# Performance work log

Hardware: AMD Instinct MI355X
Metric: run time of the kernel (lower is better)

## Reference

```python
import jax, jax.numpy as jnp
import numpy as np
from jax import lax

NUM_SAMPLES = 16
EPSILON = 1e-08
CHUNK = 1024  # tile size for the reverse NN search (matches torch batch_size)


def _cdist(a, b):
    # Euclidean distance matrix [Na, Nb] via gemm form, numerically floored for sqrt.
    d2 = (a * a).sum(-1)[:, None] + (b * b).sum(-1)[None, :] - 2.0 * (a @ b.T)
    return jnp.sqrt(jnp.maximum(d2, 1e-12))


def setup_inputs() -> dict:
    key = jax.random.key(0)
    k = jax.random.split(key, 6)
    N, F, M, G = 16384, 16384, 4096, 8192
    return {
        "original_vertices": jax.random.normal(k[0], (N, 3), dtype=jnp.float32),
        "original_faces": jax.random.randint(k[1], (F, 3), 0, N),
        "simplified_vertices": jax.random.normal(k[2], (M, 3), dtype=jnp.float32),
        "simplified_faces": jax.random.randint(k[3], (G, 3), 0, M),
        "face_probabilities": jax.random.uniform(k[4], (G,), dtype=jnp.float32),
        "r1": jax.random.uniform(k[5], (G, NUM_SAMPLES, 1), dtype=jnp.float32),
        "r2": jax.random.uniform(jax.random.fold_in(key, 7), (G, NUM_SAMPLES, 1), dtype=jnp.float32),
    }


def reference(original_vertices, original_faces, simplified_vertices,
              simplified_faces, face_probabilities, r1, r2):
    G = simplified_faces.shape[0]
    probs = face_probabilities[:G]  # pad/slice to num simplified faces (identity here)

    # ---- forward term: simplified barycenters -> nearest original barycenter ----
    orig_bary = original_vertices[original_faces].mean(axis=1)      # [F,3]
    simp_bary = simplified_vertices[simplified_faces].mean(axis=1)  # [G,3]
    min_d = _cdist(simp_bary, orig_bary).min(axis=1)                # [G]
    forward_term = (probs * min_d).sum() + 1e-4 * (1.0 - probs).sum()

    # ---- reverse term: sample points on simplified faces, NN to original verts ----
    sqrt_r1 = jnp.sqrt(r1)
    u = 1.0 - sqrt_r1
    v = sqrt_r1 * (1.0 - r2)
    w = sqrt_r1 * r2
    fv = simplified_vertices[simplified_faces]  # [G,3,3]
    pts = (u * fv[:, None, 0] + v * fv[:, None, 1] + w * fv[:, None, 2]).reshape(-1, 3)

    total = pts.shape[0]  # G * NUM_SAMPLES, divisible by CHUNK
    vsq = (original_vertices * original_vertices).sum(-1)  # [N]

    def chunk_min(p):  # p: [CHUNK, 3]
        d2 = (p * p).sum(-1)[:, None] + vsq[None, :] - 2.0 * (p @ original_vertices.T)
        return jnp.sqrt(jnp.maximum(d2, 1e-12)).min(axis=1)

    mins = lax.map(chunk_min, pts.reshape(total // CHUNK, CHUNK, 3)).reshape(-1)
    max_dist = mins.max() + EPSILON
    scaled = mins / max_dist * 0.1
    probs_exp = jnp.repeat(probs, NUM_SAMPLES)
    reverse_term = (probs_exp * scaled).sum()

    return forward_term + reverse_term
```

## Files before the change

### kernel.cpp

```cpp
#include <hip/hip_runtime.h>
#include <math.h>

constexpr int N_V  = 16384;
constexpr int N_F  = 16384;
constexpr int G_F  = 8192;
constexpr int NS   = 16;
constexpr int NPTS = G_F * NS;

constexpr int MB    = 2;
constexpr int CT    = 16;

typedef _Float16 half8 __attribute__((ext_vector_type(8)));
typedef float    f32x16 __attribute__((ext_vector_type(16)));

constexpr int F4_ACC   = 0;
constexpr int F4_SB    = 1;
constexpr int F4_PTS   = F4_SB + G_F;
constexpr int F4_PKV   = F4_PTS + NPTS;
constexpr int F4_PKO   = F4_PKV + 32768;
constexpr int F4_TOTAL = F4_PKO + 32768;
constexpr int WS_MINF  = F4_TOTAL * 4;
constexpr int WS_MINR  = WS_MINF + G_F;

__device__ __forceinline__ f32x16 mfma16(half8 a, half8 b, f32x16 c) {
  return __builtin_amdgcn_mfma_f32_32x32x16_f16(a, b, c, 0, 0, 0);
}

__device__ __forceinline__ void pack_target(float x, float y, float z, float sq,
                                            half8* __restrict__ pk, int tile, int n) {
  float ax = -2.0f*x, ay = -2.0f*y, az = -2.0f*z;
  _Float16 hx = (_Float16)ax, hy = (_Float16)ay, hz = (_Float16)az, hw = (_Float16)sq;
  _Float16 lx = (_Float16)(ax - (float)hx), ly = (_Float16)(ay - (float)hy);
  _Float16 lz = (_Float16)(az - (float)hz), lw = (_Float16)(sq - (float)hw);
  half8 h0; h0[0]=hx; h0[1]=hy; h0[2]=hz; h0[3]=hw; h0[4]=lx; h0[5]=ly; h0[6]=lz; h0[7]=lw;
  half8 h1; h1[0]=hx; h1[1]=hy; h1[2]=hz; h1[3]=hw;
  h1[4]=(_Float16)0.0f; h1[5]=(_Float16)0.0f; h1[6]=(_Float16)0.0f; h1[7]=(_Float16)0.0f;
  pk[(size_t)tile*64 + n]      = h0;
  pk[(size_t)tile*64 + 32 + n] = h1;
}

__global__ void k_prep(const float* __restrict__ ov, const int* __restrict__ of,
                       const float* __restrict__ sv, const int* __restrict__ sf,
                       const float* __restrict__ r1, const float* __restrict__ r2,
                       unsigned int* __restrict__ ws, float4* __restrict__ ws4) {
  int i = blockIdx.x * blockDim.x + threadIdx.x;
  if (i < 4) ws[i] = 0u;
  ws[WS_MINR + i] = 0x7f800000u;

  {
    int g = i >> 4;
    int a = sf[3*g], b = sf[3*g+1], c = sf[3*g+2];
    float sr = sqrtf(r1[i]);
    float u = 1.0f - sr;
    float v = sr * (1.0f - r2[i]);
    float w = sr * r2[i];
    float px = u*sv[3*a]   + v*sv[3*b]   + w*sv[3*c];
    float py = u*sv[3*a+1] + v*sv[3*b+1] + w*sv[3*c+1];
    float pz = u*sv[3*a+2] + v*sv[3*b+2] + w*sv[3*c+2];
    (ws4 + F4_PTS)[i] = make_float4(px, py, pz, fmaf(px, px, fmaf(py, py, pz*pz)));
  }
  if (i < G_F) {
    ws[WS_MINF + i] = 0x7f800000u;
    int a = sf[3*i], b = sf[3*i+1], c = sf[3*i+2];
    float x = (sv[3*a] + sv[3*b] + sv[3*c]) * (1.0f/3.0f);
    float y = (sv[3*a+1] + sv[3*b+1] + sv[3*c+1]) * (1.0f/3.0f);
    float z = (sv[3*a+2] + sv[3*b+2] + sv[3*c+2]) * (1.0f/3.0f);
    (ws4 + F4_SB)[i] = make_float4(x, y, z, fmaf(x, x, fmaf(y, y, z*z)));
  }
  if (i < N_V) {
    float x = ov[3*i], y = ov[3*i+1], z = ov[3*i+2];
    pack_target(x, y, z, fmaf(x, x, fmaf(y, y, z*z)),
                (half8*)(ws4 + F4_PKV), i >> 5, i & 31);
  }
  if (i < N_F) {
    int a = of[3*i], b = of[3*i+1], c = of[3*i+2];
    float x = (ov[3*a] + ov[3*b] + ov[3*c]) * (1.0f/3.0f);
    float y = (ov[3*a+1] + ov[3*b+1] + ov[3*c+1]) * (1.0f/3.0f);
    float z = (ov[3*a+2] + ov[3*b+2] + ov[3*c+2]) * (1.0f/3.0f);
    pack_target(x, y, z, fmaf(x, x, fmaf(y, y, z*z)),
                (half8*)(ws4 + F4_PKO), i >> 5, i & 31);
  }
}

__global__ __launch_bounds__(256, 4) void k_min(
    const float4* __restrict__ q4r, const half8* __restrict__ pkr,
    unsigned int* __restrict__ mUr,
    const float4* __restrict__ q4f, const half8* __restrict__ pkf,
    unsigned int* __restrict__ mUf, int nchunks) {
  __shared__ half8 sB[2][CT * 64];
  int lane  = threadIdx.x & 63;
  int wave  = threadIdx.x >> 6;
  int half_ = lane >> 5;
  int m     = lane & 31;

  const bool isFwd = (blockIdx.x >= (unsigned)(NPTS/256));
  const float4*  q4   = isFwd ? q4f : q4r;
  const half8*   pk   = isFwd ? pkf : pkr;
  unsigned int*  minU = isFwd ? mUf : mUr;
  int bx    = isFwd ? (int)blockIdx.x - NPTS/256 : (int)blockIdx.x;
  int qbase = bx * 256 + wave * (32 * MB);
  int tbase = blockIdx.y * nchunks * CT;

  {
    const half8* src = pk + (size_t)(tbase + wave) * 64 + lane;
    #pragma unroll
    for (int j = 0; j < CT/4; ++j) {
      __builtin_amdgcn_global_load_lds(
          (const __attribute__((address_space(1))) unsigned int*)(src + (size_t)j*256),
          (__attribute__((address_space(3))) unsigned int*)&sB[0][(wave + 4*j) * 64],
          16, 0, 0);
    }
  }

  half8 afrag[MB];
  float psq[MB];
  #pragma unroll
  for (int mb = 0; mb < MB; ++mb) {
    float4 q = q4[qbase + mb*32 + m];
    psq[mb] = q.w;
    _Float16 hx = (_Float16)q.x, hy = (_Float16)q.y, hz = (_Float16)q.z;
    half8 a;
    if (half_ == 0) {
      a[0]=hx; a[1]=hy; a[2]=hz; a[3]=(_Float16)1.0f;
      a[4]=hx; a[5]=hy; a[6]=hz; a[7]=(_Float16)1.0f;
    } else {
      a[0]=(_Float16)(q.x-(float)hx); a[1]=(_Float16)(q.y-(float)hy);
      a[2]=(_Float16)(q.z-(float)hz); a[3]=(_Float16)0.0f;
      a[4]=(_Float16)0.0f; a[5]=(_Float16)0.0f; a[6]=(_Float16)0.0f; a[7]=(_Float16)0.0f;
    }
    afrag[mb] = a;
  }

  float inf = __uint_as_float(0x7f800000u);
  f32x16 rm0, rm1, zro;
  #pragma unroll
  for (int r = 0; r < 16; ++r) { rm0[r] = inf; rm1[r] = inf; zro[r] = 0.0f; }

  for (int ch = 0; ch < nchunks; ++ch) {
    const int b = ch & 1;
    __syncthreads();
    if (ch + 1 < nchunks) {
      const half8* src = pk + (size_t)(tbase + (ch+1)*CT + wave) * 64 + lane;
      #pragma unroll
      for (int j = 0; j < CT/4; ++j) {
        __builtin_amdgcn_global_load_lds(
            (const __attribute__((address_space(1))) unsigned int*)(src + (size_t)j*256),
            (__attribute__((address_space(3))) unsigned int*)&sB[b^1][(wave + 4*j) * 64],
            16, 0, 0);
      }
    }

    #pragma unroll
    for (int t = 0; t < CT; t += 2) {
      half8 cA = sB[b][t*64 + lane];
      half8 cB = sB[b][t*64 + 64 + lane];
      f32x16 dA = mfma16(afrag[0], cA, zro);
      f32x16 dB = mfma16(afrag[0], cB, zro);
      #pragma unroll
      for (int r = 0; r < 16; ++r)
        rm0[r] = fminf(fminf(rm0[r], dA[r]), dB[r]);
      dA = mfma16(afrag[1], cA, zro);
      dB = mfma16(afrag[1], cB, zro);
      #pragma unroll
      for (int r = 0; r < 16; ++r)
        rm1[r] = fminf(fminf(rm1[r], dA[r]), dB[r]);
    }
  }

  #pragma unroll
  for (int mb = 0; mb < MB; ++mb) {
    #pragma unroll
    for (int r = 0; r < 16; ++r) {
      float v = (mb == 0) ? rm0[r] : rm1[r];
      v = fminf(v, __shfl_xor(v, 1, 64));
      v = fminf(v, __shfl_xor(v, 2, 64));
      v = fminf(v, __shfl_xor(v, 4, 64));
      v = fminf(v, __shfl_xor(v, 8, 64));
      v = fminf(v, __shfl_xor(v, 16, 64));
      int row = (r & 3) + 8*(r >> 2) + 4*half_;
      if (m == row) {
        float d2 = fmaxf(psq[mb] + v, 0.0f);
        atomicMin(&minU[qbase + mb*32 + m], __float_as_uint(d2));
      }
    }
  }
}

__device__ __forceinline__ float waveSum(float v) {
  #pragma unroll
  for (int o = 32; o > 0; o >>= 1) v += __shfl_down(v, o, 64);
  return v;
}
__device__ __forceinline__ float waveMax(float v) {
  #pragma unroll
  for (int o = 32; o > 0; o >>= 1) v = fmaxf(v, __shfl_down(v, o, 64));
  return v;
}

__global__ void k_reduce(const float* __restrict__ probs, const float* __restrict__ minf,
                         const float* __restrict__ minr, float* __restrict__ acc) {
  int tid = blockIdx.x * blockDim.x + threadIdx.x;
  int stride = gridDim.x * blockDim.x;
  float sf = 0.0f, sr = 0.0f, mx = 0.0f;
  for (int i = tid; i < NPTS; i += stride) {
    float d = sqrtf(fmaxf(minr[i], 1e-12f));
    sr = fmaf(probs[i >> 4], d, sr);
    mx = fmaxf(mx, d);
    if (i < G_F) {
      float df = sqrtf(fmaxf(minf[i], 1e-12f));
      sf = fmaf(probs[i], df, sf);
      sf = fmaf(1e-4f, 1.0f - probs[i], sf);
    }
  }
  __shared__ float lf[4], lr[4], lm[4];
  int lane = threadIdx.x & 63, wid = threadIdx.x >> 6;
  sf = waveSum(sf); sr = waveSum(sr); mx = waveMax(mx);
  if (lane == 0) { lf[wid] = sf; lr[wid] = sr; lm[wid] = mx; }
  __syncthreads();
  if (wid == 0) {
    float a = (lane < 4) ? lf[lane] : 0.0f;
    float b = (lane < 4) ? lr[lane] : 0.0f;
    float c = (lane < 4) ? lm[lane] : 0.0f;
    a = waveSum(a); b = waveSum(b); c = waveMax(c);
    if (lane == 0) {
      atomicAdd(&acc[0], a);
      atomicAdd(&acc[1], b);
      atomicMax((unsigned int*)&acc[2], __float_as_uint(c));
    }
  }
}

__global__ void k_final(const float* __restrict__ acc, float* __restrict__ out) {
  float maxd = acc[2] + 1e-8f;
  out[0] = acc[0] + acc[1] * 0.1f / maxd;
}

extern "C" void kernel_launch(void* const* d_in, const int* in_sizes, int n_in,
                              void* d_out, int out_size, void* d_ws, size_t ws_size,
                              hipStream_t stream) {
  const float* ov    = (const float*)d_in[0];
  const int*   of    = (const int*)  d_in[1];
  const float* sv    = (const float*)d_in[2];
  const int*   sfc   = (const int*)  d_in[3];
  const float* probs = (const float*)d_in[4];
  const float* r1    = (const float*)d_in[5];
  const float* r2    = (const float*)d_in[6];
  float*  ws  = (float*)d_ws;
  float4* ws4 = (float4*)d_ws;
  float*  out = (float*)d_out;

  float*        acc   = ws;
  float4*       sb4   = ws4 + F4_SB;
  float4*       pts4  = ws4 + F4_PTS;
  half8*        pkV   = (half8*)(ws4 + F4_PKV);
  half8*        pkO   = (half8*)(ws4 + F4_PKO);
  unsigned int* minfU = (unsigned int*)(ws + WS_MINF);
  unsigned int* minrU = (unsigned int*)(ws + WS_MINR);
  const float*  minfF = ws + WS_MINF;
  const float*  minrF = ws + WS_MINR;

  k_prep<<<NPTS/256, 256, 0, stream>>>(ov, of, sv, sfc, r1, r2,
                                       (unsigned int*)ws, ws4);
  k_min<<<dim3(NPTS/256 + G_F/256, 8), 256, 0, stream>>>(
      pts4, pkV, minrU, sb4, pkO, minfU, 4);
  k_reduce<<<256, 256, 0, stream>>>(probs, minfF, minrF, acc);
  k_final<<<1, 1, 0, stream>>>(acc, out);
}
```

Before: 167.4 us.

## Give each wave a private LDS double buffer and drop block-wide barriers

Each wave now streams its own copy of the target tiles into a per-wave LDS double buffer. It waits only on its own vector-memory counter instead of calling __syncthreads every chunk. The chunk is shrunk to 4 tiles with 16 chunks, so each block still covers the same targets. In exchange every wave issues four times as many global-to-LDS loads for duplicated data, and correctness now rests on the hand-written vmcnt waits.

```diff
diff --git a/kernel.cpp b/kernel.cpp
--- a/kernel.cpp
+++ b/kernel.cpp
@@ -7,8 +7,8 @@
 constexpr int NS   = 16;
 constexpr int NPTS = G_F * NS;
 
-constexpr int MB    = 2;
-constexpr int CT    = 16;
+constexpr int MB = 2;
+constexpr int CT = 4;
 
 typedef _Float16 half8 __attribute__((ext_vector_type(8)));
 typedef float    f32x16 __attribute__((ext_vector_type(16)));
@@ -87,7 +87,7 @@
     unsigned int* __restrict__ mUr,
     const float4* __restrict__ q4f, const half8* __restrict__ pkf,
     unsigned int* __restrict__ mUf, int nchunks) {
-  __shared__ half8 sB[2][CT * 64];
+  __shared__ half8 sW[4][2][CT * 64];
   int lane  = threadIdx.x & 63;
   int wave  = threadIdx.x >> 6;
   int half_ = lane >> 5;
@@ -101,15 +101,14 @@
   int qbase = bx * 256 + wave * (32 * MB);
   int tbase = blockIdx.y * nchunks * CT;
 
-  {
-    const half8* src = pk + (size_t)(tbase + wave) * 64 + lane;
-    #pragma unroll
-    for (int j = 0; j < CT/4; ++j) {
-      __builtin_amdgcn_global_load_lds(
-          (const __attribute__((address_space(1))) unsigned int*)(src + (size_t)j*256),
-          (__attribute__((address_space(3))) unsigned int*)&sB[0][(wave + 4*j) * 64],
-          16, 0, 0);
-    }
+  const half8* src0 = pk + (size_t)tbase * 64 + lane;
+
+  #pragma unroll
+  for (int j = 0; j < CT; ++j) {
+    __builtin_amdgcn_global_load_lds(
+        (const __attribute__((address_space(1))) unsigned int*)(src0 + j*64),
+        (__attribute__((address_space(3))) unsigned int*)&sW[wave][0][j*64],
+        16, 0, 0);
   }
 
   half8 afrag[MB];
@@ -137,23 +136,25 @@
   for (int r = 0; r < 16; ++r) { rm0[r] = inf; rm1[r] = inf; zro[r] = 0.0f; }
 
   for (int ch = 0; ch < nchunks; ++ch) {
-    const int b = ch & 1;
-    __syncthreads();
+    const int buf = ch & 1;
     if (ch + 1 < nchunks) {
-      const half8* src = pk + (size_t)(tbase + (ch+1)*CT + wave) * 64 + lane;
+      const half8* s = src0 + (size_t)((ch+1) * CT) * 64;
       #pragma unroll
-      for (int j = 0; j < CT/4; ++j) {
+      for (int j = 0; j < CT; ++j) {
         __builtin_amdgcn_global_load_lds(
-            (const __attribute__((address_space(1))) unsigned int*)(src + (size_t)j*256),
-            (__attribute__((address_space(3))) unsigned int*)&sB[b^1][(wave + 4*j) * 64],
+            (const __attribute__((address_space(1))) unsigned int*)(s + j*64),
+            (__attribute__((address_space(3))) unsigned int*)&sW[wave][buf^1][j*64],
             16, 0, 0);
       }
+      asm volatile("s_waitcnt vmcnt(4)" ::: "memory");
+    } else {
+      asm volatile("s_waitcnt vmcnt(0)" ::: "memory");
     }
 
     #pragma unroll
     for (int t = 0; t < CT; t += 2) {
-      half8 cA = sB[b][t*64 + lane];
-      half8 cB = sB[b][t*64 + 64 + lane];
+      half8 cA = sW[wave][buf][t*64 + lane];
+      half8 cB = sW[wave][buf][t*64 + 64 + lane];
       f32x16 dA = mfma16(afrag[0], cA, zro);
       f32x16 dB = mfma16(afrag[0], cB, zro);
       #pragma unroll
@@ -262,7 +263,7 @@
   k_prep<<<NPTS/256, 256, 0, stream>>>(ov, of, sv, sfc, r1, r2,
                                        (unsigned int*)ws, ws4);
   k_min<<<dim3(NPTS/256 + G_F/256, 8), 256, 0, stream>>>(
-      pts4, pkV, minrU, sb4, pkO, minfU, 4);
+      pts4, pkV, minrU, sb4, pkO, minfU, 16);
   k_reduce<<<256, 256, 0, stream>>>(probs, minfF, minrF, acc);
   k_final<<<1, 1, 0, stream>>>(acc, out);
 }
```

Result: slower. 178.1 us (+6.3%).
